# Performance work log

Hardware: AMD Instinct MI355X
Metric: run time of the kernel (lower is better)

## Reference

```python
import jax, jax.numpy as jnp
import numpy as np

N = 100000      # nodes
E = 1600000     # edges
D = 64          # latent_dim
H = 4           # num_heads
HID = 256       # hidden_dim of omics generators
OMICS = [20000, 1881, 27000]  # mrna, mirna, methylation output dims


def _layer_norm(x, w, b, eps=1e-5):
    m = jnp.mean(x, axis=-1, keepdims=True)
    v = jnp.var(x, axis=-1, keepdims=True)
    return (x - m) * jax.lax.rsqrt(v + eps) * w + b


def setup_inputs() -> dict:
    key = jax.random.key(0)
    ks = jax.random.split(key, 64)
    ki = iter(range(64))
    def g(shape, scale=0.05):
        return jax.random.normal(ks[next(ki)], shape, dtype=jnp.float32) * scale
    inp = {
        'latent_vectors': jax.random.normal(ks[next(ki)], (N, D), dtype=jnp.float32),
        'edge_index': jax.random.randint(ks[next(ki)], (2, E), 0, N, dtype=jnp.int32),
        # attention graph constructor (weights stored as [in,out], i.e. torch W^T)
        'wq': g((D, D)), 'bq': jnp.zeros((D,), jnp.float32),
        'wk': g((D, D)), 'bk': jnp.zeros((D,), jnp.float32),
        'wv': g((D, D)), 'bv': jnp.zeros((D,), jnp.float32),
        'ln0_w': jnp.ones((D,), jnp.float32), 'ln0_b': jnp.zeros((D,), jnp.float32),
        # two residual GCN layers
        'gcn1_w': g((D, D)), 'gcn1_b': jnp.zeros((D,), jnp.float32),
        'ln1_w': jnp.ones((D,), jnp.float32), 'ln1_b': jnp.zeros((D,), jnp.float32),
        'gcn2_w': g((D, D)), 'gcn2_b': jnp.zeros((D,), jnp.float32),
        'ln2_w': jnp.ones((D,), jnp.float32), 'ln2_b': jnp.zeros((D,), jnp.float32),
    }
    for j, od in enumerate(OMICS):
        inp[f'gw1_{j}'] = g((D, HID))
        inp[f'gb1_{j}'] = jnp.zeros((HID,), jnp.float32)
        inp[f'gw2_{j}'] = g((HID, od))
        inp[f'gb2_{j}'] = jnp.zeros((od,), jnp.float32)
    return inp


def _gcn(x, row, col, dis, w, b):
    h = x @ w                                   # [N, D]
    norm = (dis[row] * dis[col])[:, None]       # [E+N, 1]
    agg = jax.ops.segment_sum(h[row] * norm, col, num_segments=N)
    return agg + b


def reference(latent_vectors, wq, bq, wk, bk, wv, bv, ln0_w, ln0_b,
              gcn1_w, gcn1_b, ln1_w, ln1_b, gcn2_w, gcn2_b, ln2_w, ln2_b,
              gw1_0, gb1_0, gw2_0, gb2_0,
              gw1_1, gb1_1, gw2_1, gb2_1,
              gw1_2, gb1_2, gw2_2, gb2_2,
              edge_index):
    Dh = D // H
    # AttentionGraphConstructor (faithful: seq dim = 1, attention mixes heads)
    q = (latent_vectors @ wq + bq).reshape(N, 1, H, Dh)
    k = (latent_vectors @ wk + bk).reshape(N, 1, H, Dh)
    v = (latent_vectors @ wv + bv).reshape(N, 1, H, Dh)
    scores = jnp.einsum('nsid,nsjd->nsij', q, k) / (Dh ** 0.5)  # [N,1,H,H]
    attn = jax.nn.softmax(scores, axis=-1)
    out = jnp.einsum('nsij,nsjd->nsid', attn, v)                # [N,1,H,Dh]
    x = _layer_norm(out.transpose(0, 2, 1, 3).reshape(N, D), ln0_w, ln0_b)
    # GCN normalization with self-loops: D^-1/2 (A+I) D^-1/2
    loops = jnp.arange(N, dtype=edge_index.dtype)
    row = jnp.concatenate([edge_index[0], loops])
    col = jnp.concatenate([edge_index[1], loops])
    deg = jax.ops.segment_sum(jnp.ones_like(col, dtype=x.dtype), col, num_segments=N)
    dis = jnp.where(deg > 0, jax.lax.rsqrt(jnp.maximum(deg, 1e-12)), 0.0)
    for gw, gb, lw, lb in ((gcn1_w, gcn1_b, ln1_w, ln1_b),
                           (gcn2_w, gcn2_b, ln2_w, ln2_b)):
        h = _gcn(x, row, col, dis, gw, gb)
        x = _layer_norm(x + h, lw, lb)        # residual (in==out dims)
    # per-omics MLP generators on x[i] (dropout = identity in eval)
    gens = ((gw1_0, gb1_0, gw2_0, gb2_0),
            (gw1_1, gb1_1, gw2_1, gb2_1),
            (gw1_2, gb1_2, gw2_2, gb2_2))
    outs = []
    for i, (w1, b1, w2, b2) in enumerate(gens):
        xi = x[i:i + 1]                        # [1, D]
        hi = jax.nn.relu(xi @ w1 + b1)
        outs.append(hi @ w2 + b2)              # [1, od]
    return jnp.concatenate(outs, axis=-1)      # [1, sum(OMICS)]
```

## Files before the change

### kernel.cpp

```cpp
#include <hip/hip_runtime.h>

#define NN 100000
#define NE 1600000
#define HIDN 256
#define OD0 20000
#define OD1 1881
#define OD2 27000
#define OUT_TOTAL (OD0 + OD1 + OD2)

#define MAXL1 8192
#define MAXS1 1024
#define MAXL2 65536
#define MAXS2 8192

__device__ __forceinline__ float wave_sum64(float v) {
#pragma unroll
    for (int off = 32; off >= 1; off >>= 1) v += __shfl_xor(v, off, 64);
    return v;
}

__global__ void k_scan1(const int* __restrict__ erow, const int* __restrict__ ecol,
                        int* __restrict__ cnts, int2* __restrict__ L1) {
    int i = blockIdx.x * blockDim.x + threadIdx.x;
    if (i >= NE / 4) return;
    int4 c4 = ((const int4*)ecol)[i];
    int cs[4] = {c4.x, c4.y, c4.z, c4.w};
#pragma unroll
    for (int u = 0; u < 4; u++) {
        if (cs[u] < 3) {
            int idx = atomicAdd(&cnts[0], 1);
            if (idx < MAXL1) L1[idx] = make_int2(erow[i * 4 + u], cs[u]);
        }
    }
}

__global__ void k_s1(int* __restrict__ cnts, const int2* __restrict__ L1,
                     int* __restrict__ flag1, int* __restrict__ slot1, int* __restrict__ S1) {
    int i = blockIdx.x * blockDim.x + threadIdx.x;
    int nl1 = min(cnts[0], MAXL1);
    int n = -1;
    if (i < 3) n = i;
    else if (i - 3 < nl1) n = L1[i - 3].x;
    if (n < 0) return;
    if (atomicExch(&flag1[n], 1) == 0) {
        int s = atomicAdd(&cnts[1], 1);
        if (s < MAXS1) { slot1[n] = s; S1[s] = n; }
    }
}

__global__ void k_scan2(const int* __restrict__ erow, const int* __restrict__ ecol,
                        const int* __restrict__ flag1, int* __restrict__ cnts, int2* __restrict__ L2) {
    int i = blockIdx.x * blockDim.x + threadIdx.x;
    if (i >= NE / 4) return;
    int4 c4 = ((const int4*)ecol)[i];
    int cs[4] = {c4.x, c4.y, c4.z, c4.w};
#pragma unroll
    for (int u = 0; u < 4; u++) {
        if (flag1[cs[u]]) {
            int idx = atomicAdd(&cnts[2], 1);
            if (idx < MAXL2) L2[idx] = make_int2(erow[i * 4 + u], cs[u]);
        }
    }
}

__global__ void k_s2(int* __restrict__ cnts, const int2* __restrict__ L2, const int* __restrict__ S1,
                     int* __restrict__ slot2, int* __restrict__ S2) {
    int i = blockIdx.x * blockDim.x + threadIdx.x;
    int nl2 = min(cnts[2], MAXL2);
    int ns1 = min(cnts[1], MAXS1);
    int n = -1;
    if (i < nl2) n = L2[i].x;
    else if (i - nl2 < ns1) n = S1[i - nl2];
    if (n < 0) return;
    if (atomicCAS(&slot2[n], -1, -2) == -1) {
        int s = atomicAdd(&cnts[3], 1);
        if (s < MAXS2) { slot2[n] = s; S2[s] = n; }
    }
}

__global__ void k_deg2(const int* __restrict__ ecol, const int* __restrict__ slot2,
                       int* __restrict__ degc) {
    int i = blockIdx.x * blockDim.x + threadIdx.x;
    if (i >= NE / 4) return;
    int4 c4 = ((const int4*)ecol)[i];
    int cs[4] = {c4.x, c4.y, c4.z, c4.w};
#pragma unroll
    for (int u = 0; u < 4; u++) {
        int s = slot2[cs[u]];
        if (s >= 0 && s < MAXS2) atomicAdd(&degc[s], 1);
    }
}

#define X0_GRID 192
__global__ __launch_bounds__(256) void k_x0h1(
        const int* __restrict__ cnts, const int* __restrict__ S2,
        const float* __restrict__ latent,
        const float* __restrict__ wq, const float* __restrict__ bq,
        const float* __restrict__ wk, const float* __restrict__ bk,
        const float* __restrict__ wv, const float* __restrict__ bv,
        const float* __restrict__ ln0w, const float* __restrict__ ln0b,
        const float* __restrict__ g1w,
        float* __restrict__ x0c, float* __restrict__ h1c) {
    __shared__ float lw[3 * 4096];
    __shared__ float lsm[5 * 64];
    int t = threadIdx.x;
    {
        const float4* s0 = (const float4*)wq;
        const float4* s1 = (const float4*)wk;
        const float4* s2 = (const float4*)wv;
        float4* d0 = (float4*)&lw[0];
        float4* d1 = (float4*)&lw[4096];
        float4* d2 = (float4*)&lw[8192];
        for (int i = t; i < 1024; i += 256) { d0[i] = s0[i]; d1[i] = s1[i]; d2[i] = s2[i]; }
        if (t < 64) {
            lsm[t] = bq[t]; lsm[64 + t] = bk[t]; lsm[128 + t] = bv[t];
            lsm[192 + t] = ln0w[t]; lsm[256 + t] = ln0b[t];
        }
    }
    __syncthreads();
    int lane = t & 63, w = t >> 6;
    int nS2 = min(cnts[3], MAXS2);
    for (int s = blockIdx.x * 4 + w; s < nS2; s += X0_GRID * 4) {
        int n = S2[s];
        float xv = latent[n * 64 + lane];
        float aq = lsm[lane], ak = lsm[64 + lane], av = lsm[128 + lane];
#pragma unroll
        for (int j = 0; j < 64; j++) {
            float xj = __shfl(xv, j, 64);
            aq = fmaf(xj, lw[j * 64 + lane], aq);
            ak = fmaf(xj, lw[4096 + j * 64 + lane], ak);
            av = fmaf(xj, lw[8192 + j * 64 + lane], av);
        }
        int d = lane & 15;
        float sj[4];
#pragma unroll
        for (int j = 0; j < 4; j++) {
            float kv = __shfl(ak, (j << 4) | d, 64);
            float p = aq * kv;
            p += __shfl_xor(p, 1, 64); p += __shfl_xor(p, 2, 64);
            p += __shfl_xor(p, 4, 64); p += __shfl_xor(p, 8, 64);
            sj[j] = p * 0.25f;
        }
        float mx = fmaxf(fmaxf(sj[0], sj[1]), fmaxf(sj[2], sj[3]));
        float e0 = expf(sj[0] - mx), e1 = expf(sj[1] - mx);
        float e2 = expf(sj[2] - mx), e3 = expf(sj[3] - mx);
        float inv = 1.f / (e0 + e1 + e2 + e3);
        float at[4] = {e0 * inv, e1 * inv, e2 * inv, e3 * inv};
        float o = 0.f;
#pragma unroll
        for (int j = 0; j < 4; j++) {
            float vv = __shfl(av, (j << 4) | d, 64);
            o = fmaf(at[j], vv, o);
        }
        float sum = wave_sum64(o), sq = wave_sum64(o * o);
        float mean = sum * (1.f / 64.f);
        float var = sq * (1.f / 64.f) - mean * mean;
        float x0 = (o - mean) * rsqrtf(var + 1e-5f) * lsm[192 + lane] + lsm[256 + lane];
        x0c[s * 64 + lane] = x0;
        float h = 0.f;
#pragma unroll
        for (int j = 0; j < 64; j++) {
            float xj = __shfl(x0, j, 64);
            h = fmaf(xj, g1w[j * 64 + lane], h);
        }
        h1c[s * 64 + lane] = h;
    }
}

__global__ void k_agg1(const int* __restrict__ cnts, const int2* __restrict__ L2,
                       const int* __restrict__ S1, const int* __restrict__ slot1,
                       const int* __restrict__ slot2, const int* __restrict__ degc,
                       const float* __restrict__ h1c, float* __restrict__ agg1c) {
    int lane = threadIdx.x;
    int nl2 = min(cnts[2], MAXL2);
    int ns1 = min(cnts[1], MAXS1);
    for (int e = blockIdx.x; e < nl2 + ns1; e += gridDim.x) {
        int r, c;
        if (e < nl2) { r = L2[e].x; c = L2[e].y; }
        else { r = c = S1[e - nl2]; }
        int sr2 = slot2[r], sc2 = slot2[c], sc1 = slot1[c];
        if (sr2 < 0 || sr2 >= MAXS2 || sc2 < 0 || sc2 >= MAXS2 || sc1 < 0 || sc1 >= MAXS1) continue;
        float wgt = rsqrtf((float)(degc[sr2] + 1)) * rsqrtf((float)(degc[sc2] + 1));
        atomicAdd(&agg1c[sc1 * 64 + lane], h1c[sr2 * 64 + lane] * wgt);
    }
}

__global__ void k_x1h2(const int* __restrict__ cnts, const int* __restrict__ S1,
                       const int* __restrict__ slot2, const float* __restrict__ x0c,
                       const float* __restrict__ agg1c, const float* __restrict__ gb,
                       const float* __restrict__ lnw, const float* __restrict__ lnb,
                       const float* __restrict__ g2w,
                       float* __restrict__ x1c, float* __restrict__ h2c) {
    int lane = threadIdx.x;
    int ns1 = min(cnts[1], MAXS1);
    for (int s = blockIdx.x; s < ns1; s += gridDim.x) {
        int n = S1[s];
        int s2 = slot2[n];
        if (s2 < 0 || s2 >= MAXS2) continue;
        float v = x0c[s2 * 64 + lane] + agg1c[s * 64 + lane] + gb[lane];
        float sum = wave_sum64(v), sq = wave_sum64(v * v);
        float mean = sum * (1.f / 64.f);
        float var = sq * (1.f / 64.f) - mean * mean;
        float x1 = (v - mean) * rsqrtf(var + 1e-5f) * lnw[lane] + lnb[lane];
        x1c[s * 64 + lane] = x1;
        float h = 0.f;
#pragma unroll
        for (int j = 0; j < 64; j++) {
            float xj = __shfl(x1, j, 64);
            h = fmaf(xj, g2w[j * 64 + lane], h);
        }
        h2c[s * 64 + lane] = h;
    }
}

__global__ __launch_bounds__(256) void k_tail(
        const int* __restrict__ cnts, const int2* __restrict__ L1,
        const int* __restrict__ slot1, const int* __restrict__ slot2,
        const int* __restrict__ degc, const float* __restrict__ h2c,
        const float* __restrict__ x1c, const float* __restrict__ g2b,
        const float* __restrict__ lnw, const float* __restrict__ lnb,
        const float* __restrict__ w10, const float* __restrict__ b10,
        const float* __restrict__ w11, const float* __restrict__ b11,
        const float* __restrict__ w12, const float* __restrict__ b12,
        float* __restrict__ hg) {
    __shared__ float aggL[192], lx2[192];
    int t = threadIdx.x, lane = t & 63, w = t >> 6;
    if (t < 192) aggL[t] = 0.f;
    __syncthreads();
    int nl1 = min(cnts[0], MAXL1);
    for (int e = w; e < nl1 + 3; e += 4) {
        int r, c;
        if (e < nl1) { r = L1[e].x; c = L1[e].y; }
        else { r = c = e - nl1; }
        int sr1 = slot1[r], sr2 = slot2[r], sc2 = slot2[c];
        if (sr1 < 0 || sr1 >= MAXS1 || sr2 < 0 || sr2 >= MAXS2 || sc2 < 0 || sc2 >= MAXS2) continue;
        float wgt = rsqrtf((float)(degc[sr2] + 1)) * rsqrtf((float)(degc[sc2] + 1));
        atomicAdd(&aggL[c * 64 + lane], h2c[sr1 * 64 + lane] * wgt);
    }
    __syncthreads();
    if (w < 3) {
        int s1 = slot1[w];
        float v = x1c[s1 * 64 + lane] + aggL[w * 64 + lane] + g2b[lane];
        float sum = wave_sum64(v), sq = wave_sum64(v * v);
        float mean = sum * (1.f / 64.f);
        float var = sq * (1.f / 64.f) - mean * mean;
        lx2[w * 64 + lane] = (v - mean) * rsqrtf(var + 1e-5f) * lnw[lane] + lnb[lane];
    }
    __syncthreads();
    const float* W1[3] = {w10, w11, w12};
    const float* B1[3] = {b10, b11, b12};
#pragma unroll
    for (int gi = 0; gi < 3; gi++) {
        float acc = B1[gi][t];
#pragma unroll
        for (int j = 0; j < 64; j++) acc = fmaf(lx2[gi * 64 + j], W1[gi][j * 256 + t], acc);
        hg[gi * 256 + t] = fmaxf(acc, 0.f);
    }
}

__global__ __launch_bounds__(256) void k_out(const float* __restrict__ hg,
        const float* __restrict__ w20, const float* __restrict__ b20,
        const float* __restrict__ w21, const float* __restrict__ b21,
        const float* __restrict__ w22, const float* __restrict__ b22,
        float* __restrict__ out) {
    __shared__ float lh[768];
    __shared__ float part[256];
    int t = threadIdx.x;
    lh[t] = hg[t]; lh[t + 256] = hg[t + 256]; lh[t + 512] = hg[t + 512];
    __syncthreads();
    int tx = t & 63, ty = t >> 6;
    int o = blockIdx.x * 64 + tx;
    int gi = -1, jj = 0, od = 1;
    const float* w2 = w20;
    if (o < OD0)                 { gi = 0; jj = o;             od = OD0; w2 = w20; }
    else if (o < OD0 + OD1)      { gi = 1; jj = o - OD0;       od = OD1; w2 = w21; }
    else if (o < OUT_TOTAL)      { gi = 2; jj = o - OD0 - OD1; od = OD2; w2 = w22; }
    float acc = 0.f;
    if (gi >= 0) {
        const float* h = &lh[gi * 256 + ty * 64];
        const float* wp = &w2[(size_t)(ty * 64) * od + jj];
#pragma unroll 16
        for (int k = 0; k < 64; k++) acc = fmaf(h[k], wp[(size_t)k * od], acc);
    }
    part[t] = acc;
    __syncthreads();
    if (t < 64 && gi >= 0) {
        float r = part[t] + part[t + 64] + part[t + 128] + part[t + 192];
        const float* b2 = (gi == 0) ? b20 : (gi == 1) ? b21 : b22;
        out[o] = r + b2[jj];
    }
}

extern "C" void kernel_launch(void* const* d_in, const int* in_sizes, int n_in,
                              void* d_out, int out_size, void* d_ws, size_t ws_size,
                              hipStream_t stream) {
    (void)in_sizes; (void)n_in; (void)out_size; (void)ws_size;
    const float* latent = (const float*)d_in[0];
    const int*   edges  = (const int*)d_in[1];
    const float* wq  = (const float*)d_in[2];
    const float* bq  = (const float*)d_in[3];
    const float* wk  = (const float*)d_in[4];
    const float* bk  = (const float*)d_in[5];
    const float* wv  = (const float*)d_in[6];
    const float* bv  = (const float*)d_in[7];
    const float* ln0w = (const float*)d_in[8];
    const float* ln0b = (const float*)d_in[9];
    const float* g1w  = (const float*)d_in[10];
    const float* g1b  = (const float*)d_in[11];
    const float* ln1w = (const float*)d_in[12];
    const float* ln1b = (const float*)d_in[13];
    const float* g2w  = (const float*)d_in[14];
    const float* g2b  = (const float*)d_in[15];
    const float* ln2w = (const float*)d_in[16];
    const float* ln2b = (const float*)d_in[17];
    const float* gw1_0 = (const float*)d_in[18];
    const float* gb1_0 = (const float*)d_in[19];
    const float* gw2_0 = (const float*)d_in[20];
    const float* gb2_0 = (const float*)d_in[21];
    const float* gw1_1 = (const float*)d_in[22];
    const float* gb1_1 = (const float*)d_in[23];
    const float* gw2_1 = (const float*)d_in[24];
    const float* gb2_1 = (const float*)d_in[25];
    const float* gw1_2 = (const float*)d_in[26];
    const float* gb1_2 = (const float*)d_in[27];
    const float* gw2_2 = (const float*)d_in[28];
    const float* gb2_2 = (const float*)d_in[29];

    char* p = (char*)d_ws;
    auto alloc = [&](size_t bytes) { char* r = p; p += (bytes + 255) & ~(size_t)255; return r; };
    int*   cnts  = (int*)alloc(64 * 4);
    int*   flag1 = (int*)alloc((size_t)NN * 4);
    int*   degc  = (int*)alloc((size_t)MAXS2 * 4);
    float* agg1c = (float*)alloc((size_t)MAXS1 * 64 * 4);
    char*  zero_end = p;
    int*   slot1 = (int*)alloc((size_t)NN * 4);
    int*   slot2 = (int*)alloc((size_t)NN * 4);
    char*  ff_end = p;
    int2*  L1    = (int2*)alloc((size_t)MAXL1 * 8);
    int*   S1    = (int*)alloc((size_t)MAXS1 * 4);
    int2*  L2    = (int2*)alloc((size_t)MAXL2 * 8);
    int*   S2    = (int*)alloc((size_t)MAXS2 * 4);
    float* x0c   = (float*)alloc((size_t)MAXS2 * 64 * 4);
    float* h1c   = (float*)alloc((size_t)MAXS2 * 64 * 4);
    float* x1c   = (float*)alloc((size_t)MAXS1 * 64 * 4);
    float* h2c   = (float*)alloc((size_t)MAXS1 * 64 * 4);
    float* hg    = (float*)alloc(3 * HIDN * 4);

    const int* erow = edges;
    const int* ecol = edges + NE;

    hipMemsetAsync(cnts, 0, (size_t)(zero_end - (char*)cnts), stream);
    hipMemsetAsync(slot1, 0xFF, (size_t)(ff_end - (char*)slot1), stream);

    const int SCAN_GRID = (NE / 4 + 255) / 256;
    k_scan1<<<SCAN_GRID, 256, 0, stream>>>(erow, ecol, cnts, L1);
    k_s1<<<(MAXL1 + 3 + 255) / 256, 256, 0, stream>>>(cnts, L1, flag1, slot1, S1);
    k_scan2<<<SCAN_GRID, 256, 0, stream>>>(erow, ecol, flag1, cnts, L2);
    k_s2<<<(MAXL2 + MAXS1 + 255) / 256, 256, 0, stream>>>(cnts, L2, S1, slot2, S2);
    k_deg2<<<SCAN_GRID, 256, 0, stream>>>(ecol, slot2, degc);
    k_x0h1<<<X0_GRID, 256, 0, stream>>>(cnts, S2, latent, wq, bq, wk, bk, wv, bv,
                                        ln0w, ln0b, g1w, x0c, h1c);
    k_agg1<<<256, 64, 0, stream>>>(cnts, L2, S1, slot1, slot2, degc, h1c, agg1c);
    k_x1h2<<<64, 64, 0, stream>>>(cnts, S1, slot2, x0c, agg1c, g1b, ln1w, ln1b, g2w, x1c, h2c);
    k_tail<<<1, 256, 0, stream>>>(cnts, L1, slot1, slot2, degc, h2c, x1c, g2b, ln2w, ln2b,
                                  gw1_0, gb1_0, gw1_1, gb1_1, gw1_2, gb1_2, hg);
    k_out<<<(OUT_TOTAL + 63) / 64, 256, 0, stream>>>(hg, gw2_0, gb2_0, gw2_1, gb2_1,
                                                     gw2_2, gb2_2, (float*)d_out);
}
```

Measured before the change: 85.00 us.

## Fuse graph frontier discovery into scans with bitmasks and merge GCN stages

Frontier membership for hop-1 and hop-2 nodes is now built inside the edge scans, using atomicOr on compact bitmasks instead of separate set-building kernels over large flag arrays. Degree counting is folded into the attention/x0 kernel. The first-layer aggregation and layer-norm now run inside the single-block tail kernel using shared memory. Both memsets are replaced by one small zeroing kernel, and MAXS1 drops to 112. The aim is fewer launches and less memset and scan traffic. The cost is more serial work in the one-block tail, and slot arrays are no longer reset to -1, so correctness relies on only reading slots of nodes that are set members.

Result: slower. 219.0 us (+157.7%).

```diff
diff --git a/kernel.cpp b/kernel.cpp
--- a/kernel.cpp
+++ b/kernel.cpp
@@ -9,92 +9,85 @@
 #define OUT_TOTAL (OD0 + OD1 + OD2)
 
 #define MAXL1 8192
-#define MAXS1 1024
+#define MAXS1 112
 #define MAXL2 65536
 #define MAXS2 8192
 
+#define MASKW 3200
+
 __device__ __forceinline__ float wave_sum64(float v) {
 #pragma unroll
     for (int off = 32; off >= 1; off >>= 1) v += __shfl_xor(v, off, 64);
     return v;
 }
 
-__global__ void k_scan1(const int* __restrict__ erow, const int* __restrict__ ecol,
-                        int* __restrict__ cnts, int2* __restrict__ L1) {
+__device__ __forceinline__ void insert_set(unsigned* mask, int* cnt, int cap,
+                                           int* slot, int* list, int n) {
+    unsigned bit = 1u << (n & 31);
+    unsigned old = atomicOr(&mask[n >> 5], bit);
+    if (!(old & bit)) {
+        int s = atomicAdd(cnt, 1);
+        if (s < cap) { slot[n] = s; list[s] = n; }
+    }
+}
+
+__global__ void k_init(int4* base, int n4) {
     int i = blockIdx.x * blockDim.x + threadIdx.x;
-    if (i >= NE / 4) return;
-    int4 c4 = ((const int4*)ecol)[i];
-    int cs[4] = {c4.x, c4.y, c4.z, c4.w};
-#pragma unroll
-    for (int u = 0; u < 4; u++) {
-        if (cs[u] < 3) {
-            int idx = atomicAdd(&cnts[0], 1);
-            if (idx < MAXL1) L1[idx] = make_int2(erow[i * 4 + u], cs[u]);
-        }
-    }
-}
-
-__global__ void k_s1(int* __restrict__ cnts, const int2* __restrict__ L1,
-                     int* __restrict__ flag1, int* __restrict__ slot1, int* __restrict__ S1) {
-    int i = blockIdx.x * blockDim.x + threadIdx.x;
-    int nl1 = min(cnts[0], MAXL1);
-    int n = -1;
-    if (i < 3) n = i;
-    else if (i - 3 < nl1) n = L1[i - 3].x;
-    if (n < 0) return;
-    if (atomicExch(&flag1[n], 1) == 0) {
-        int s = atomicAdd(&cnts[1], 1);
-        if (s < MAXS1) { slot1[n] = s; S1[s] = n; }
-    }
-}
-
-__global__ void k_scan2(const int* __restrict__ erow, const int* __restrict__ ecol,
-                        const int* __restrict__ flag1, int* __restrict__ cnts, int2* __restrict__ L2) {
-    int i = blockIdx.x * blockDim.x + threadIdx.x;
-    if (i >= NE / 4) return;
-    int4 c4 = ((const int4*)ecol)[i];
-    int cs[4] = {c4.x, c4.y, c4.z, c4.w};
-#pragma unroll
-    for (int u = 0; u < 4; u++) {
-        if (flag1[cs[u]]) {
-            int idx = atomicAdd(&cnts[2], 1);
-            if (idx < MAXL2) L2[idx] = make_int2(erow[i * 4 + u], cs[u]);
-        }
-    }
-}
-
-__global__ void k_s2(int* __restrict__ cnts, const int2* __restrict__ L2, const int* __restrict__ S1,
-                     int* __restrict__ slot2, int* __restrict__ S2) {
-    int i = blockIdx.x * blockDim.x + threadIdx.x;
-    int nl2 = min(cnts[2], MAXL2);
+    int4 z = make_int4(0, 0, 0, 0);
+    for (; i < n4; i += gridDim.x * blockDim.x) base[i] = z;
+}
+
+__global__ __launch_bounds__(256) void k_scan1(
+        const int* __restrict__ erow, const int* __restrict__ ecol,
+        int* __restrict__ cnts, unsigned* __restrict__ mask1,
+        int* __restrict__ slot1, int* __restrict__ S1, int2* __restrict__ L1) {
+    int gid = blockIdx.x * blockDim.x + threadIdx.x;
+    if (gid < 3) insert_set(mask1, &cnts[1], MAXS1, slot1, S1, gid);
+    for (int i = gid; i < NE / 4; i += gridDim.x * blockDim.x) {
+        int4 c4 = ((const int4*)ecol)[i];
+        int cs[4] = {c4.x, c4.y, c4.z, c4.w};
+#pragma unroll
+        for (int u = 0; u < 4; u++) {
+            if (cs[u] < 3) {
+                int r = erow[i * 4 + u];
+                int idx = atomicAdd(&cnts[0], 1);
+                if (idx < MAXL1) L1[idx] = make_int2(r, cs[u]);
+                insert_set(mask1, &cnts[1], MAXS1, slot1, S1, r);
+            }
+        }
+    }
+}
+
+__global__ __launch_bounds__(256) void k_scan2(
+        const int* __restrict__ erow, const int* __restrict__ ecol,
+        int* __restrict__ cnts, const unsigned* __restrict__ mask1,
+        unsigned* __restrict__ mask2, int* __restrict__ slot2,
+        int* __restrict__ S2, const int* __restrict__ S1, int2* __restrict__ L2) {
+    int gid = blockIdx.x * blockDim.x + threadIdx.x;
     int ns1 = min(cnts[1], MAXS1);
-    int n = -1;
-    if (i < nl2) n = L2[i].x;
-    else if (i - nl2 < ns1) n = S1[i - nl2];
-    if (n < 0) return;
-    if (atomicCAS(&slot2[n], -1, -2) == -1) {
-        int s = atomicAdd(&cnts[3], 1);
-        if (s < MAXS2) { slot2[n] = s; S2[s] = n; }
-    }
-}
-
-__global__ void k_deg2(const int* __restrict__ ecol, const int* __restrict__ slot2,
-                       int* __restrict__ degc) {
-    int i = blockIdx.x * blockDim.x + threadIdx.x;
-    if (i >= NE / 4) return;
-    int4 c4 = ((const int4*)ecol)[i];
-    int cs[4] = {c4.x, c4.y, c4.z, c4.w};
-#pragma unroll
-    for (int u = 0; u < 4; u++) {
-        int s = slot2[cs[u]];
-        if (s >= 0 && s < MAXS2) atomicAdd(&degc[s], 1);
-    }
-}
-
-#define X0_GRID 192
-__global__ __launch_bounds__(256) void k_x0h1(
-        const int* __restrict__ cnts, const int* __restrict__ S2,
-        const float* __restrict__ latent,
+    if (gid < ns1) insert_set(mask2, &cnts[3], MAXS2, slot2, S2, S1[gid]);
+    for (int i = gid; i < NE / 4; i += gridDim.x * blockDim.x) {
+        int4 c4 = ((const int4*)ecol)[i];
+        int cs[4] = {c4.x, c4.y, c4.z, c4.w};
+#pragma unroll
+        for (int u = 0; u < 4; u++) {
+            int c = cs[u];
+            if (mask1[c >> 5] & (1u << (c & 31))) {
+                int r = erow[i * 4 + u];
+                int idx = atomicAdd(&cnts[2], 1);
+                if (idx < MAXL2) L2[idx] = make_int2(r, c);
+                insert_set(mask2, &cnts[3], MAXS2, slot2, S2, r);
+            }
+        }
+    }
+}
+
+#define DX_GRID 256
+__global__ __launch_bounds__(256) void k_degx0(
+        const int* __restrict__ cnts, const int* __restrict__ ecol,
+        const unsigned* __restrict__ mask2, const int* __restrict__ slot2,
+        int* __restrict__ degc,
+        const int* __restrict__ S2, const float* __restrict__ latent,
         const float* __restrict__ wq, const float* __restrict__ bq,
         const float* __restrict__ wk, const float* __restrict__ bk,
         const float* __restrict__ wv, const float* __restrict__ bv,
@@ -102,8 +95,8 @@
         const float* __restrict__ g1w,
         float* __restrict__ x0c, float* __restrict__ h1c) {
     __shared__ float lw[3 * 4096];
-    __shared__ float lsm[5 * 64];
-    int t = threadIdx.x;
+    int t = threadIdx.x, b = blockIdx.x;
+    int gid = b * 256 + t;
     {
         const float4* s0 = (const float4*)wq;
         const float4* s1 = (const float4*)wk;
@@ -112,18 +105,26 @@
         float4* d1 = (float4*)&lw[4096];
         float4* d2 = (float4*)&lw[8192];
         for (int i = t; i < 1024; i += 256) { d0[i] = s0[i]; d1[i] = s1[i]; d2[i] = s2[i]; }
-        if (t < 64) {
-            lsm[t] = bq[t]; lsm[64 + t] = bk[t]; lsm[128 + t] = bv[t];
-            lsm[192 + t] = ln0w[t]; lsm[256 + t] = ln0b[t];
-        }
-    }
-    __syncthreads();
-    int lane = t & 63, w = t >> 6;
+    }
+    for (int i = gid; i < NE / 4; i += DX_GRID * 256) {
+        int4 c4 = ((const int4*)ecol)[i];
+        int cs[4] = {c4.x, c4.y, c4.z, c4.w};
+#pragma unroll
+        for (int u = 0; u < 4; u++) {
+            int c = cs[u];
+            if (mask2[c >> 5] & (1u << (c & 31))) {
+                int s = slot2[c];
+                if ((unsigned)s < MAXS2) atomicAdd(&degc[s], 1);
+            }
+        }
+    }
+    __syncthreads();
+    int lane = t & 63, wid = t >> 6;
     int nS2 = min(cnts[3], MAXS2);
-    for (int s = blockIdx.x * 4 + w; s < nS2; s += X0_GRID * 4) {
+    for (int s = b * 4 + wid; s < nS2; s += DX_GRID * 4) {
         int n = S2[s];
         float xv = latent[n * 64 + lane];
-        float aq = lsm[lane], ak = lsm[64 + lane], av = lsm[128 + lane];
+        float aq = bq[lane], ak = bk[lane], av = bv[lane];
 #pragma unroll
         for (int j = 0; j < 64; j++) {
             float xj = __shfl(xv, j, 64);
@@ -136,10 +137,10 @@
 #pragma unroll
         for (int j = 0; j < 4; j++) {
             float kv = __shfl(ak, (j << 4) | d, 64);
-            float p = aq * kv;
-            p += __shfl_xor(p, 1, 64); p += __shfl_xor(p, 2, 64);
-            p += __shfl_xor(p, 4, 64); p += __shfl_xor(p, 8, 64);
-            sj[j] = p * 0.25f;
+            float pp = aq * kv;
+            pp += __shfl_xor(pp, 1, 64); pp += __shfl_xor(pp, 2, 64);
+            pp += __shfl_xor(pp, 4, 64); pp += __shfl_xor(pp, 8, 64);
+            sj[j] = pp * 0.25f;
         }
         float mx = fmaxf(fmaxf(sj[0], sj[1]), fmaxf(sj[2], sj[3]));
         float e0 = expf(sj[0] - mx), e1 = expf(sj[1] - mx);
@@ -155,7 +156,7 @@
         float sum = wave_sum64(o), sq = wave_sum64(o * o);
         float mean = sum * (1.f / 64.f);
         float var = sq * (1.f / 64.f) - mean * mean;
-        float x0 = (o - mean) * rsqrtf(var + 1e-5f) * lsm[192 + lane] + lsm[256 + lane];
+        float x0 = (o - mean) * rsqrtf(var + 1e-5f) * ln0w[lane] + ln0b[lane];
         x0c[s * 64 + lane] = x0;
         float h = 0.f;
 #pragma unroll
@@ -167,84 +168,74 @@
     }
 }
 
-__global__ void k_agg1(const int* __restrict__ cnts, const int2* __restrict__ L2,
-                       const int* __restrict__ S1, const int* __restrict__ slot1,
-                       const int* __restrict__ slot2, const int* __restrict__ degc,
-                       const float* __restrict__ h1c, float* __restrict__ agg1c) {
-    int lane = threadIdx.x;
-    int nl2 = min(cnts[2], MAXL2);
-    int ns1 = min(cnts[1], MAXS1);
-    for (int e = blockIdx.x; e < nl2 + ns1; e += gridDim.x) {
-        int r, c;
-        if (e < nl2) { r = L2[e].x; c = L2[e].y; }
-        else { r = c = S1[e - nl2]; }
-        int sr2 = slot2[r], sc2 = slot2[c], sc1 = slot1[c];
-        if (sr2 < 0 || sr2 >= MAXS2 || sc2 < 0 || sc2 >= MAXS2 || sc1 < 0 || sc1 >= MAXS1) continue;
-        float wgt = rsqrtf((float)(degc[sr2] + 1)) * rsqrtf((float)(degc[sc2] + 1));
-        atomicAdd(&agg1c[sc1 * 64 + lane], h1c[sr2 * 64 + lane] * wgt);
-    }
-}
-
-__global__ void k_x1h2(const int* __restrict__ cnts, const int* __restrict__ S1,
-                       const int* __restrict__ slot2, const float* __restrict__ x0c,
-                       const float* __restrict__ agg1c, const float* __restrict__ gb,
-                       const float* __restrict__ lnw, const float* __restrict__ lnb,
-                       const float* __restrict__ g2w,
-                       float* __restrict__ x1c, float* __restrict__ h2c) {
-    int lane = threadIdx.x;
-    int ns1 = min(cnts[1], MAXS1);
-    for (int s = blockIdx.x; s < ns1; s += gridDim.x) {
-        int n = S1[s];
-        int s2 = slot2[n];
-        if (s2 < 0 || s2 >= MAXS2) continue;
-        float v = x0c[s2 * 64 + lane] + agg1c[s * 64 + lane] + gb[lane];
-        float sum = wave_sum64(v), sq = wave_sum64(v * v);
-        float mean = sum * (1.f / 64.f);
-        float var = sq * (1.f / 64.f) - mean * mean;
-        float x1 = (v - mean) * rsqrtf(var + 1e-5f) * lnw[lane] + lnb[lane];
-        x1c[s * 64 + lane] = x1;
-        float h = 0.f;
-#pragma unroll
-        for (int j = 0; j < 64; j++) {
-            float xj = __shfl(x1, j, 64);
-            h = fmaf(xj, g2w[j * 64 + lane], h);
-        }
-        h2c[s * 64 + lane] = h;
-    }
-}
-
 __global__ __launch_bounds__(256) void k_tail(
         const int* __restrict__ cnts, const int2* __restrict__ L1,
+        const int2* __restrict__ L2, const int* __restrict__ S1,
         const int* __restrict__ slot1, const int* __restrict__ slot2,
-        const int* __restrict__ degc, const float* __restrict__ h2c,
-        const float* __restrict__ x1c, const float* __restrict__ g2b,
-        const float* __restrict__ lnw, const float* __restrict__ lnb,
+        const int* __restrict__ degc,
+        const float* __restrict__ x0c, const float* __restrict__ h1c,
+        const float* __restrict__ g1b, const float* __restrict__ ln1w,
+        const float* __restrict__ ln1b, const float* __restrict__ g2w,
+        const float* __restrict__ g2b, const float* __restrict__ ln2w,
+        const float* __restrict__ ln2b,
         const float* __restrict__ w10, const float* __restrict__ b10,
         const float* __restrict__ w11, const float* __restrict__ b11,
         const float* __restrict__ w12, const float* __restrict__ b12,
         float* __restrict__ hg) {
-    __shared__ float aggL[192], lx2[192];
-    int t = threadIdx.x, lane = t & 63, w = t >> 6;
-    if (t < 192) aggL[t] = 0.f;
-    __syncthreads();
+    __shared__ float s_acc[MAXS1 * 64];
+    __shared__ float s_h2[MAXS1 * 64];
+    __shared__ float s_agg2[192], s_x2[192];
+    int t = threadIdx.x, lane = t & 63, wid = t >> 6;
     int nl1 = min(cnts[0], MAXL1);
-    for (int e = w; e < nl1 + 3; e += 4) {
+    int ns1 = min(cnts[1], MAXS1);
+    int nl2 = min(cnts[2], MAXL2);
+    for (int i = t; i < MAXS1 * 64; i += 256) s_acc[i] = 0.f;
+    if (t < 192) s_agg2[t] = 0.f;
+    __syncthreads();
+    for (int e = wid; e < nl2 + ns1; e += 4) {
         int r, c;
-        if (e < nl1) { r = L1[e].x; c = L1[e].y; }
-        else { r = c = e - nl1; }
-        int sr1 = slot1[r], sr2 = slot2[r], sc2 = slot2[c];
-        if (sr1 < 0 || sr1 >= MAXS1 || sr2 < 0 || sr2 >= MAXS2 || sc2 < 0 || sc2 >= MAXS2) continue;
+        if (e < nl2) { int2 rc = L2[e]; r = rc.x; c = rc.y; }
+        else { r = c = S1[e - nl2]; }
+        int sr2 = slot2[r], sc2 = slot2[c], sc1 = slot1[c];
+        if ((unsigned)sr2 >= MAXS2 || (unsigned)sc2 >= MAXS2 || (unsigned)sc1 >= (unsigned)ns1) continue;
         float wgt = rsqrtf((float)(degc[sr2] + 1)) * rsqrtf((float)(degc[sc2] + 1));
-        atomicAdd(&aggL[c * 64 + lane], h2c[sr1 * 64 + lane] * wgt);
-    }
-    __syncthreads();
-    if (w < 3) {
-        int s1 = slot1[w];
-        float v = x1c[s1 * 64 + lane] + aggL[w * 64 + lane] + g2b[lane];
+        atomicAdd(&s_acc[sc1 * 64 + lane], h1c[sr2 * 64 + lane] * wgt);
+    }
+    __syncthreads();
+    for (int s = wid; s < ns1; s += 4) {
+        int s2 = slot2[S1[s]];
+        float v = x0c[s2 * 64 + lane] + s_acc[s * 64 + lane] + g1b[lane];
         float sum = wave_sum64(v), sq = wave_sum64(v * v);
         float mean = sum * (1.f / 64.f);
         float var = sq * (1.f / 64.f) - mean * mean;
-        lx2[w * 64 + lane] = (v - mean) * rsqrtf(var + 1e-5f) * lnw[lane] + lnb[lane];
+        float x1 = (v - mean) * rsqrtf(var + 1e-5f) * ln1w[lane] + ln1b[lane];
+        s_acc[s * 64 + lane] = x1;
+        float h = 0.f;
+#pragma unroll
+        for (int j = 0; j < 64; j++) {
+            float xj = __shfl(x1, j, 64);
+            h = fmaf(xj, g2w[j * 64 + lane], h);
+        }
+        s_h2[s * 64 + lane] = h;
+    }
+    __syncthreads();
+    for (int e = wid; e < nl1 + 3; e += 4) {
+        int r, c;
+        if (e < nl1) { int2 rc = L1[e]; r = rc.x; c = rc.y; }
+        else { r = c = e - nl1; }
+        int sr1 = slot1[r], sr2 = slot2[r], sc2 = slot2[c];
+        if ((unsigned)sr1 >= (unsigned)ns1 || (unsigned)sr2 >= MAXS2 || (unsigned)sc2 >= MAXS2) continue;
+        float wgt = rsqrtf((float)(degc[sr2] + 1)) * rsqrtf((float)(degc[sc2] + 1));
+        atomicAdd(&s_agg2[c * 64 + lane], s_h2[sr1 * 64 + lane] * wgt);
+    }
+    __syncthreads();
+    if (wid < 3) {
+        int s1 = slot1[wid];
+        float v = s_acc[s1 * 64 + lane] + s_agg2[wid * 64 + lane] + g2b[lane];
+        float sum = wave_sum64(v), sq = wave_sum64(v * v);
+        float mean = sum * (1.f / 64.f);
+        float var = sq * (1.f / 64.f) - mean * mean;
+        s_x2[wid * 64 + lane] = (v - mean) * rsqrtf(var + 1e-5f) * ln2w[lane] + ln2b[lane];
     }
     __syncthreads();
     const float* W1[3] = {w10, w11, w12};
@@ -253,7 +244,7 @@
     for (int gi = 0; gi < 3; gi++) {
         float acc = B1[gi][t];
 #pragma unroll
-        for (int j = 0; j < 64; j++) acc = fmaf(lx2[gi * 64 + j], W1[gi][j * 256 + t], acc);
+        for (int j = 0; j < 64; j++) acc = fmaf(s_x2[gi * 64 + j], W1[gi][j * 256 + t], acc);
         hg[gi * 256 + t] = fmaxf(acc, 0.f);
     }
 }
@@ -326,43 +317,35 @@
     const float* gw2_2 = (const float*)d_in[28];
     const float* gb2_2 = (const float*)d_in[29];
 
-    char* p = (char*)d_ws;
-    auto alloc = [&](size_t bytes) { char* r = p; p += (bytes + 255) & ~(size_t)255; return r; };
-    int*   cnts  = (int*)alloc(64 * 4);
-    int*   flag1 = (int*)alloc((size_t)NN * 4);
-    int*   degc  = (int*)alloc((size_t)MAXS2 * 4);
-    float* agg1c = (float*)alloc((size_t)MAXS1 * 64 * 4);
-    char*  zero_end = p;
-    int*   slot1 = (int*)alloc((size_t)NN * 4);
-    int*   slot2 = (int*)alloc((size_t)NN * 4);
-    char*  ff_end = p;
-    int2*  L1    = (int2*)alloc((size_t)MAXL1 * 8);
-    int*   S1    = (int*)alloc((size_t)MAXS1 * 4);
-    int2*  L2    = (int2*)alloc((size_t)MAXL2 * 8);
-    int*   S2    = (int*)alloc((size_t)MAXS2 * 4);
-    float* x0c   = (float*)alloc((size_t)MAXS2 * 64 * 4);
-    float* h1c   = (float*)alloc((size_t)MAXS2 * 64 * 4);
-    float* x1c   = (float*)alloc((size_t)MAXS1 * 64 * 4);
-    float* h2c   = (float*)alloc((size_t)MAXS1 * 64 * 4);
-    float* hg    = (float*)alloc(3 * HIDN * 4);
+    char* ptr = (char*)d_ws;
+    auto alloc = [&](size_t bytes) { char* r = ptr; ptr += (bytes + 255) & ~(size_t)255; return r; };
+    int*      cnts  = (int*)alloc(64 * 4);
+    unsigned* mask1 = (unsigned*)alloc(MASKW * 4);
+    unsigned* mask2 = (unsigned*)alloc(MASKW * 4);
+    int*      degc  = (int*)alloc((size_t)MAXS2 * 4);
+    char*     zero_end = ptr;
+    int*      slot1 = (int*)alloc((size_t)NN * 4);
+    int*      slot2 = (int*)alloc((size_t)NN * 4);
+    int2*     L1    = (int2*)alloc((size_t)MAXL1 * 8);
+    int*      S1    = (int*)alloc((size_t)MAXS1 * 4);
+    int2*     L2    = (int2*)alloc((size_t)MAXL2 * 8);
+    int*      S2    = (int*)alloc((size_t)MAXS2 * 4);
+    float*    x0c   = (float*)alloc((size_t)MAXS2 * 64 * 4);
+    float*    h1c   = (float*)alloc((size_t)MAXS2 * 64 * 4);
+    float*    hg    = (float*)alloc(3 * HIDN * 4);
 
     const int* erow = edges;
     const int* ecol = edges + NE;
-
-    hipMemsetAsync(cnts, 0, (size_t)(zero_end - (char*)cnts), stream);
-    hipMemsetAsync(slot1, 0xFF, (size_t)(ff_end - (char*)slot1), stream);
+    int zero_n4 = (int)((zero_end - (char*)cnts) / 16);
 
     const int SCAN_GRID = (NE / 4 + 255) / 256;
-    k_scan1<<<SCAN_GRID, 256, 0, stream>>>(erow, ecol, cnts, L1);
-    k_s1<<<(MAXL1 + 3 + 255) / 256, 256, 0, stream>>>(cnts, L1, flag1, slot1, S1);
-    k_scan2<<<SCAN_GRID, 256, 0, stream>>>(erow, ecol, flag1, cnts, L2);
-    k_s2<<<(MAXL2 + MAXS1 + 255) / 256, 256, 0, stream>>>(cnts, L2, S1, slot2, S2);
-    k_deg2<<<SCAN_GRID, 256, 0, stream>>>(ecol, slot2, degc);
-    k_x0h1<<<X0_GRID, 256, 0, stream>>>(cnts, S2, latent, wq, bq, wk, bk, wv, bv,
-                                        ln0w, ln0b, g1w, x0c, h1c);
-    k_agg1<<<256, 64, 0, stream>>>(cnts, L2, S1, slot1, slot2, degc, h1c, agg1c);
-    k_x1h2<<<64, 64, 0, stream>>>(cnts, S1, slot2, x0c, agg1c, g1b, ln1w, ln1b, g2w, x1c, h2c);
-    k_tail<<<1, 256, 0, stream>>>(cnts, L1, slot1, slot2, degc, h2c, x1c, g2b, ln2w, ln2b,
+    k_init<<<16, 256, 0, stream>>>((int4*)cnts, zero_n4);
+    k_scan1<<<SCAN_GRID, 256, 0, stream>>>(erow, ecol, cnts, mask1, slot1, S1, L1);
+    k_scan2<<<SCAN_GRID, 256, 0, stream>>>(erow, ecol, cnts, mask1, mask2, slot2, S2, S1, L2);
+    k_degx0<<<DX_GRID, 256, 0, stream>>>(cnts, ecol, mask2, slot2, degc, S2, latent,
+                                         wq, bq, wk, bk, wv, bv, ln0w, ln0b, g1w, x0c, h1c);
+    k_tail<<<1, 256, 0, stream>>>(cnts, L1, L2, S1, slot1, slot2, degc, x0c, h1c,
+                                  g1b, ln1w, ln1b, g2w, g2b, ln2w, ln2b,
                                   gw1_0, gb1_0, gw1_1, gb1_1, gw1_2, gb1_2, hg);
     k_out<<<(OUT_TOTAL + 63) / 64, 256, 0, stream>>>(hg, gw2_0, gb2_0, gw2_1, gb2_1,
                                                      gw2_2, gb2_2, (float*)d_out);
```
